# Optimization experiments

Measured on AMD Instinct MI355X. Metric: run time of the kernel, lower is better.

The kernel has to match this reference:

```python
import jax, jax.numpy as jnp
import numpy as np

N_POINTS = 16384
N_TOPICS = 2
N_PAIRS = 65536


def setup_inputs() -> dict:
    key = jax.random.key(0)
    ks = jax.random.split(key, 8)
    pij = jax.random.uniform(ks[0], (N_PAIRS,), dtype=jnp.float32, minval=1e-6, maxval=1.0)
    i = jax.random.randint(ks[1], (N_PAIRS,), 0, N_POINTS, dtype=jnp.int64 if jax.config.jax_enable_x64 else jnp.int32)
    j = jax.random.randint(ks[2], (N_PAIRS,), 0, N_POINTS, dtype=jnp.int64 if jax.config.jax_enable_x64 else jnp.int32)
    mu_w = jax.random.normal(ks[3], (N_POINTS, N_TOPICS), dtype=jnp.float32)
    lv_w = jax.random.normal(ks[4], (N_POINTS, N_TOPICS), dtype=jnp.float32)
    eps_full = jax.random.normal(ks[5], (N_POINTS, N_TOPICS), dtype=jnp.float32)
    eps_i = jax.random.normal(ks[6], (N_PAIRS, N_TOPICS), dtype=jnp.float32)
    eps_j = jax.random.normal(ks[7], (N_PAIRS, N_TOPICS), dtype=jnp.float32)
    return {"pij": pij, "i": i, "j": j, "mu_w": mu_w, "lv_w": lv_w,
            "eps_full": eps_full, "eps_i": eps_i, "eps_j": eps_j}


def _reparam(mu, logvar, eps):
    # z = eps * exp(0.5*logvar) + mu ; kld = -0.5 * sum(1 + logvar - mu^2 - exp(logvar))
    z = eps * jnp.exp(0.5 * logvar) + mu
    kld = -0.5 * jnp.sum(1.0 + logvar - mu * mu - jnp.exp(logvar))
    return z, kld


def reference(pij, i, j, mu_w, lv_w, eps_full, eps_i, eps_j):
    pij = pij.astype(jnp.float32)
    # full-table reparametrized embedding
    x, loss_kldrp = _reparam(mu_w, lv_w, eps_full)  # [N, D]
    # pairwise squared distances via gram trick (same math as expand/sub/pow/sum)
    x2 = jnp.sum(x * x, axis=1)  # [N]
    dkl2 = jnp.maximum(x2[:, None] + x2[None, :] - 2.0 * (x @ x.T), 0.0)  # [N, N]
    n_diagonal = x.shape[0]
    part = jnp.sum(1.0 / (1.0 + dkl2)) - n_diagonal  # scalar normalizer
    # per-pair reparametrized embeddings (fresh noise each call, as in torch)
    xi, _ = _reparam(mu_w[i], lv_w[i], eps_i)  # [P, D]
    xj, _ = _reparam(mu_w[j], lv_w[j], eps_j)  # [P, D]
    num = 1.0 / (1.0 + jnp.sum((xi - xj) ** 2, axis=1))  # [P]
    qij = num / part
    loss_kld = pij * (jnp.log(pij) - jnp.log(qij))
    return jnp.sum(loss_kld) + loss_kldrp * 1e-7
```

## Files before the change

kernel.cpp:

```cpp
#include <hip/hip_runtime.h>

#define NPTS   16384
#define NPAIRS 65536


__device__ inline float waveReduceF(float v) {
#pragma unroll
    for (int o = 32; o > 0; o >>= 1) v += __shfl_down(v, o, 64);
    return v;
}

__global__ __launch_bounds__(64) void k_prep(
        const float2* __restrict__ mu, const float2* __restrict__ lv,
        const float2* __restrict__ ef,
        const float* __restrict__ pij, const int* __restrict__ ii,
        const int* __restrict__ jj,
        const float2* __restrict__ ei, const float2* __restrict__ ej,
        float2* __restrict__ xt,
        double* __restrict__ kldPart, double* __restrict__ s1Part,
        double* __restrict__ s2Part) {
    int b = blockIdx.x;
    int lane = threadIdx.x;
    if (b < NPTS / 64) {
        int i = b * 64 + lane;
        float2 m = mu[i], l = lv[i], e = ef[i];
        float x0 = fmaf(e.x, expf(0.5f * l.x), m.x);
        float x1 = fmaf(e.y, expf(0.5f * l.y), m.y);
        xt[i] = make_float2(x0, x1);
        float k = (1.0f + l.x - m.x * m.x - expf(l.x))
                + (1.0f + l.y - m.y * m.y - expf(l.y));
        k = waveReduceF(k);
        if (lane == 0) kldPart[b] = (double)k;
    } else {
        int p = (b - NPTS / 64) * 64 + lane;
        float pv = pij[p];
        int a = ii[p], bb = jj[p];
        float2 ma = mu[a], la = lv[a], ea = ei[p];
        float2 mb = mu[bb], lb = lv[bb], eb = ej[p];
        float xa0 = fmaf(ea.x, expf(0.5f * la.x), ma.x);
        float xa1 = fmaf(ea.y, expf(0.5f * la.y), ma.y);
        float xb0 = fmaf(eb.x, expf(0.5f * lb.x), mb.x);
        float xb1 = fmaf(eb.y, expf(0.5f * lb.y), mb.y);
        float d0 = xa0 - xb0, d1 = xa1 - xb1;
        float dsq = fmaf(d0, d0, d1 * d1);
        float t = pv * (logf(pv) + log1pf(dsq));
        float s1 = waveReduceF(t);
        float s2 = waveReduceF(pv);
        if (lane == 0) {
            s1Part[b - NPTS / 64] = (double)s1;
            s2Part[b - NPTS / 64] = (double)s2;
        }
    }
}

__global__ __launch_bounds__(256) void k_part(
        const float2* __restrict__ xt, double* __restrict__ partPart) {
    int bx = blockIdx.x, by = blockIdx.y;
    int colBase = bx * 2048, rowBase = by * 64;
    double* slot = &partPart[by * 8 + bx];

    if (colBase + 2048 <= rowBase) {
        if (threadIdx.x == 0) *slot = 0.0;
        return;
    }
    int tid = threadIdx.x;
    float cx[8], cy[8], a[8];
    int jcol[8];
#pragma unroll
    for (int k = 0; k < 8; ++k) {
        int j = colBase + tid + k * 256;
        float2 c = xt[j];
        cx[k] = c.x; cy[k] = c.y; a[k] = 0.0f; jcol[k] = j;
    }
    float2 rv = xt[rowBase + (tid & 63)];

    if (colBase >= rowBase + 64) {
#pragma unroll 8
        for (int r = 0; r < 64; ++r) {
            float rx = __int_as_float(__builtin_amdgcn_readlane(__float_as_int(rv.x), r));
            float ry = __int_as_float(__builtin_amdgcn_readlane(__float_as_int(rv.y), r));
#pragma unroll
            for (int k = 0; k < 8; ++k) {
                float d0 = rx - cx[k], d1 = ry - cy[k];
                float e = fmaf(d1, d1, fmaf(d0, d0, 1.0f));
                a[k] += __builtin_amdgcn_rcpf(e);
            }
        }
    } else {
#pragma unroll 8
        for (int r = 0; r < 64; ++r) {
            int irow = rowBase + r;
            float rx = __int_as_float(__builtin_amdgcn_readlane(__float_as_int(rv.x), r));
            float ry = __int_as_float(__builtin_amdgcn_readlane(__float_as_int(rv.y), r));
#pragma unroll
            for (int k = 0; k < 8; ++k) {
                float d0 = rx - cx[k], d1 = ry - cy[k];
                float e = fmaf(d1, d1, fmaf(d0, d0, 1.0f));
                float v = __builtin_amdgcn_rcpf(e);
                a[k] += (jcol[k] > irow) ? v : 0.0f;
            }
        }
    }
    float s = ((a[0] + a[1]) + (a[2] + a[3])) + ((a[4] + a[5]) + (a[6] + a[7]));
    s = waveReduceF(s);
    __shared__ float ws4[4];
    if ((tid & 63) == 0) ws4[tid >> 6] = s;
    __syncthreads();
    if (tid == 0)
        *slot = ((double)ws4[0] + (double)ws4[1]) + ((double)ws4[2] + (double)ws4[3]);
}

__global__ __launch_bounds__(64) void k_final(
        const double* __restrict__ partPart, const double* __restrict__ kldPart,
        const double* __restrict__ s1Part, const double* __restrict__ s2Part,
        float* __restrict__ out) {
    int lane = threadIdx.x;
    double ps = 0.0, kld = 0.0, s1 = 0.0, s2 = 0.0;
#pragma unroll
    for (int k = 0; k < 32; ++k) ps += partPart[lane + k * 64];
#pragma unroll
    for (int k = 0; k < 4; ++k) kld += kldPart[lane + k * 64];
#pragma unroll
    for (int k = 0; k < 16; ++k) { s1 += s1Part[lane + k * 64]; s2 += s2Part[lane + k * 64]; }
#pragma unroll
    for (int o = 32; o > 0; o >>= 1) {
        ps  += __shfl_down(ps, o, 64);
        kld += __shfl_down(kld, o, 64);
        s1  += __shfl_down(s1, o, 64);
        s2  += __shfl_down(s2, o, 64);
    }
    if (lane == 0) {
        double part = 2.0 * ps;
        out[0] = (float)(s1 + s2 * log(part) - 0.5e-7 * kld);
    }
}

extern "C" void kernel_launch(void* const* d_in, const int* in_sizes, int n_in,
                              void* d_out, int out_size, void* d_ws, size_t ws_size,
                              hipStream_t stream) {
    const float*  pij = (const float*)d_in[0];
    const int*    ii  = (const int*)d_in[1];
    const int*    jj  = (const int*)d_in[2];
    const float2* mu  = (const float2*)d_in[3];
    const float2* lv  = (const float2*)d_in[4];
    const float2* ef  = (const float2*)d_in[5];
    const float2* ei  = (const float2*)d_in[6];
    const float2* ej  = (const float2*)d_in[7];
    float* out = (float*)d_out;

    char* ws = (char*)d_ws;
    float2* xt      = (float2*)ws;
    double* partPart = (double*)(ws + 131072);
    double* kldPart  = (double*)(ws + 147456);
    double* s1Part   = (double*)(ws + 149504);
    double* s2Part   = (double*)(ws + 157696);

    k_prep<<<NPTS / 64 + NPAIRS / 64, 64, 0, stream>>>(mu, lv, ef, pij, ii, jj,
                                                       ei, ej, xt, kldPart, s1Part, s2Part);
    dim3 gb(8, 256);
    k_part<<<gb, 256, 0, stream>>>(xt, partPart);
    k_final<<<1, 64, 0, stream>>>(partPart, kldPart, s1Part, s2Part, out);
}
```

Measured before the change: 125.7 us.

## Interleave columns across blocks to balance triangular pairwise sum work

The triangular pairwise-kernel sum now assigns columns to blocks in a strided pattern (column = bx + 8*index). Every block in a row band does an equal share of the remaining upper-triangle work, and fully masked column chunks are skipped at compile time through a KB template. This replaces the old layout, where blocks below the diagonal exited early and the rest did full work, which left the load uneven. The prep kernel also moves from 64-thread to 256-thread blocks, cutting the block count while keeping per-wave partial outputs.

```diff
diff --git a/kernel.cpp b/kernel.cpp
--- a/kernel.cpp
+++ b/kernel.cpp
@@ -10,7 +10,7 @@
     return v;
 }
 
-__global__ __launch_bounds__(64) void k_prep(
+__global__ __launch_bounds__(256) void k_prep(
         const float2* __restrict__ mu, const float2* __restrict__ lv,
         const float2* __restrict__ ef,
         const float* __restrict__ pij, const int* __restrict__ ii,
@@ -20,9 +20,10 @@
         double* __restrict__ kldPart, double* __restrict__ s1Part,
         double* __restrict__ s2Part) {
     int b = blockIdx.x;
-    int lane = threadIdx.x;
-    if (b < NPTS / 64) {
-        int i = b * 64 + lane;
+    int tid = threadIdx.x;
+    int wave = tid >> 6;
+    if (b < NPTS / 256) {
+        int i = b * 256 + tid;
         float2 m = mu[i], l = lv[i], e = ef[i];
         float x0 = fmaf(e.x, expf(0.5f * l.x), m.x);
         float x1 = fmaf(e.y, expf(0.5f * l.y), m.y);
@@ -30,9 +31,10 @@
         float k = (1.0f + l.x - m.x * m.x - expf(l.x))
                 + (1.0f + l.y - m.y * m.y - expf(l.y));
         k = waveReduceF(k);
-        if (lane == 0) kldPart[b] = (double)k;
+        if ((tid & 63) == 0) kldPart[b * 4 + wave] = (double)k;
     } else {
-        int p = (b - NPTS / 64) * 64 + lane;
+        int pb = b - NPTS / 256;
+        int p = pb * 256 + tid;
         float pv = pij[p];
         int a = ii[p], bb = jj[p];
         float2 ma = mu[a], la = lv[a], ea = ei[p];
@@ -46,68 +48,72 @@
         float t = pv * (logf(pv) + log1pf(dsq));
         float s1 = waveReduceF(t);
         float s2 = waveReduceF(pv);
-        if (lane == 0) {
-            s1Part[b - NPTS / 64] = (double)s1;
-            s2Part[b - NPTS / 64] = (double)s2;
+        if ((tid & 63) == 0) {
+            s1Part[pb * 4 + wave] = (double)s1;
+            s2Part[pb * 4 + wave] = (double)s2;
         }
     }
+}
+
+template<int KB>
+__device__ __forceinline__ float partBody(const float2* __restrict__ xt,
+                                          int bx, int rowBase, int tid) {
+    constexpr int NK = 8 - KB;
+    float cx[NK], cy[NK], a[NK];
+    int j0 = bx + 8 * (tid + 256 * KB);
+#pragma unroll
+    for (int m = 0; m < NK; ++m) {
+        float2 c = xt[j0 + 2048 * m];
+        cx[m] = c.x; cy[m] = c.y; a[m] = 0.0f;
+    }
+    float2 rv = xt[rowBase + (tid & 63)];
+#pragma unroll 4
+    for (int r = 0; r < 64; ++r) {
+        float rx = __int_as_float(__builtin_amdgcn_readlane(__float_as_int(rv.x), r));
+        float ry = __int_as_float(__builtin_amdgcn_readlane(__float_as_int(rv.y), r));
+        {
+            float d0 = rx - cx[0], d1 = ry - cy[0];
+            float e = fmaf(d1, d1, fmaf(d0, d0, 1.0f));
+            float v = __builtin_amdgcn_rcpf(e);
+            a[0] += (j0 > rowBase + r) ? v : 0.0f;
+        }
+#pragma unroll
+        for (int m = 1; m < NK; ++m) {
+            float d0 = rx - cx[m], d1 = ry - cy[m];
+            float e = fmaf(d1, d1, fmaf(d0, d0, 1.0f));
+            a[m] += __builtin_amdgcn_rcpf(e);
+        }
+    }
+    float s = 0.0f;
+#pragma unroll
+    for (int m = 0; m < NK; ++m) s += a[m];
+    return s;
 }
 
 __global__ __launch_bounds__(256) void k_part(
         const float2* __restrict__ xt, double* __restrict__ partPart) {
     int bx = blockIdx.x, by = blockIdx.y;
-    int colBase = bx * 2048, rowBase = by * 64;
-    double* slot = &partPart[by * 8 + bx];
-
-    if (colBase + 2048 <= rowBase) {
-        if (threadIdx.x == 0) *slot = 0.0;
-        return;
+    int rowBase = by * 64;
+    int kb = by >> 5;
+    int tid = threadIdx.x;
+    float s = 0.0f;
+    switch (kb) {
+        case 0: s = partBody<0>(xt, bx, rowBase, tid); break;
+        case 1: s = partBody<1>(xt, bx, rowBase, tid); break;
+        case 2: s = partBody<2>(xt, bx, rowBase, tid); break;
+        case 3: s = partBody<3>(xt, bx, rowBase, tid); break;
+        case 4: s = partBody<4>(xt, bx, rowBase, tid); break;
+        case 5: s = partBody<5>(xt, bx, rowBase, tid); break;
+        case 6: s = partBody<6>(xt, bx, rowBase, tid); break;
+        default: s = partBody<7>(xt, bx, rowBase, tid); break;
     }
-    int tid = threadIdx.x;
-    float cx[8], cy[8], a[8];
-    int jcol[8];
-#pragma unroll
-    for (int k = 0; k < 8; ++k) {
-        int j = colBase + tid + k * 256;
-        float2 c = xt[j];
-        cx[k] = c.x; cy[k] = c.y; a[k] = 0.0f; jcol[k] = j;
-    }
-    float2 rv = xt[rowBase + (tid & 63)];
-
-    if (colBase >= rowBase + 64) {
-#pragma unroll 8
-        for (int r = 0; r < 64; ++r) {
-            float rx = __int_as_float(__builtin_amdgcn_readlane(__float_as_int(rv.x), r));
-            float ry = __int_as_float(__builtin_amdgcn_readlane(__float_as_int(rv.y), r));
-#pragma unroll
-            for (int k = 0; k < 8; ++k) {
-                float d0 = rx - cx[k], d1 = ry - cy[k];
-                float e = fmaf(d1, d1, fmaf(d0, d0, 1.0f));
-                a[k] += __builtin_amdgcn_rcpf(e);
-            }
-        }
-    } else {
-#pragma unroll 8
-        for (int r = 0; r < 64; ++r) {
-            int irow = rowBase + r;
-            float rx = __int_as_float(__builtin_amdgcn_readlane(__float_as_int(rv.x), r));
-            float ry = __int_as_float(__builtin_amdgcn_readlane(__float_as_int(rv.y), r));
-#pragma unroll
-            for (int k = 0; k < 8; ++k) {
-                float d0 = rx - cx[k], d1 = ry - cy[k];
-                float e = fmaf(d1, d1, fmaf(d0, d0, 1.0f));
-                float v = __builtin_amdgcn_rcpf(e);
-                a[k] += (jcol[k] > irow) ? v : 0.0f;
-            }
-        }
-    }
-    float s = ((a[0] + a[1]) + (a[2] + a[3])) + ((a[4] + a[5]) + (a[6] + a[7]));
     s = waveReduceF(s);
     __shared__ float ws4[4];
     if ((tid & 63) == 0) ws4[tid >> 6] = s;
     __syncthreads();
     if (tid == 0)
-        *slot = ((double)ws4[0] + (double)ws4[1]) + ((double)ws4[2] + (double)ws4[3]);
+        partPart[by * 8 + bx] =
+            ((double)ws4[0] + (double)ws4[1]) + ((double)ws4[2] + (double)ws4[3]);
 }
 
 __global__ __launch_bounds__(64) void k_final(
@@ -149,14 +155,14 @@
     float* out = (float*)d_out;
 
     char* ws = (char*)d_ws;
-    float2* xt      = (float2*)ws;
+    float2* xt       = (float2*)ws;
     double* partPart = (double*)(ws + 131072);
     double* kldPart  = (double*)(ws + 147456);
     double* s1Part   = (double*)(ws + 149504);
     double* s2Part   = (double*)(ws + 157696);
 
-    k_prep<<<NPTS / 64 + NPAIRS / 64, 64, 0, stream>>>(mu, lv, ef, pij, ii, jj,
-                                                       ei, ej, xt, kldPart, s1Part, s2Part);
+    k_prep<<<NPTS / 256 + NPAIRS / 256, 256, 0, stream>>>(mu, lv, ef, pij, ii, jj,
+                                                          ei, ej, xt, kldPart, s1Part, s2Part);
     dim3 gb(8, 256);
     k_part<<<gb, 256, 0, stream>>>(xt, partPart);
     k_final<<<1, 64, 0, stream>>>(partPart, kldPart, s1Part, s2Part, out);
```

Measured after the change: 105.4 us. -16.1%, faster.
